# Kernel tuning notes

Measured on AMD Instinct MI355X. Metric: run time of the kernel, lower is better.

The kernel has to match this reference:

```python
import jax, jax.numpy as jnp
import numpy as np

BLOCKS = 32
BLOCK_SIZE = 8
CONV_SHAPES = [(128, 96), (128, 128), (96, 128)] * 2  # per-block conv (out,in) list


def build_conv_meta():
    meta = []
    w_total = 0
    b_total = 0
    for _ in range(BLOCKS):
        for oc, ic in CONV_SHAPES:
            meta.append((oc, ic, w_total, b_total))
            w_total += oc * ic * 9
            b_total += oc
    return meta, w_total, b_total

CONV_META, W_TOTAL, B_TOTAL = build_conv_meta()


def build_program():
    ops = [[0, 0, 0, 0], [1, 0, 0, 0], [2, 0, 0, 0]]
    for blk in range(BLOCKS):
        ops.append([3, 0, 1, 2])  # SPLIT r0 -> (r1, r2)
        for rnd in range(2):
            ci = blk * 6 + rnd * 3
            ops += [
                [4, 3, 2, ci],      # r3 = conv(r2)        128<-96
                [5, 3, 3, 0],       # r3 = relu(r3)
                [4, 3, 3, ci + 1],  # r3 = conv(r3)        128<-128
                [5, 3, 3, 0],       # r3 = relu(r3)
                [4, 3, 3, ci + 2],  # r3 = conv(r3)        96<-128
                [6, 1, 1, 3],       # r1 = r1 + r3
                [9, 1, 2, 0],       # swap(r1, r2)  (Feistel)
            ]
        ops += [[7, 0, 1, 2],       # r0 = concat(r1, r2)
                [8, 0, 0, blk]]     # r0 = mix[blk] @ r0 (1x1 conv)
    return np.array(ops, dtype=np.int64)


def space_to_depth(x, blk):
    b, c, h, w = x.shape
    x = x.reshape(b, c, h // blk, blk, w // blk, blk)
    x = jnp.transpose(x, (0, 1, 3, 5, 2, 4))
    return x.reshape(b, c * blk * blk, h // blk, w // blk)


def conv3x3(x, w, b):
    y = jax.lax.conv_general_dilated(
        x, w, window_strides=(1, 1), padding=[(1, 1), (1, 1)],
        dimension_numbers=('NCHW', 'OIHW', 'NCHW'))
    return y + b[None, :, None, None]


def run_program(x, mu, sigma, w_flat, b_flat, m, perm, ops):
    regs = [x, None, None, None, None]
    for row in np.asarray(ops):
        op, a, b, c = (int(v) for v in row)
        if op == 0:  # AFFINE
            regs[a] = (regs[a] - mu[None, :, None, None]) / sigma[None, :, None, None]
        elif op == 1:  # PERM: gather along flattened HW per channel
            bs, ch, h, w = regs[a].shape
            v = regs[a].reshape(bs, ch, h * w)
            regs[a] = jnp.take_along_axis(v, perm[None], axis=2).reshape(bs, ch, h, w)
        elif op == 2:  # S2D
            regs[a] = space_to_depth(regs[a], BLOCK_SIZE)
        elif op == 3:  # SPLIT
            regs[b], regs[c] = jnp.split(regs[a], 2, axis=1)
        elif op == 4:  # CONV (weights sliced from flat buffer, static offsets)
            oc, ic, woff, boff = CONV_META[c]
            w = w_flat[woff:woff + oc * ic * 9].reshape(oc, ic, 3, 3)
            bb = b_flat[boff:boff + oc]
            regs[a] = conv3x3(regs[b], w, bb)
        elif op == 5:  # RELU
            regs[a] = jax.nn.relu(regs[b])
        elif op == 6:  # ADD
            regs[a] = regs[b] + regs[c]
        elif op == 7:  # CONCAT
            regs[a] = jnp.concatenate([regs[b], regs[c]], axis=1)
        elif op == 8:  # MIX: 1x1 conv with 192x192 orthogonal matrix
            regs[a] = jnp.einsum('oc,bchw->bohw', m[c], regs[b])
        elif op == 9:  # SWAP
            regs[a], regs[b] = regs[b], regs[a]
        else:
            raise ValueError('bad op')
    return regs[0]


def setup_inputs() -> dict:
    key = jax.random.key(0)
    k_x, k_w, k_b = jax.random.split(key, 3)
    rng = np.random.default_rng(0)

    x = jax.random.normal(k_x, (8, 3, 256, 256), dtype=jnp.float32)
    mu = jnp.full((3,), 0.45, dtype=jnp.float32)
    sigma = jnp.full((3,), 0.2, dtype=jnp.float32)
    # conv weights ~ He-ish scale so activations stay bounded across 64 Feistel rounds
    w_flat = jax.random.normal(k_w, (W_TOTAL,), dtype=jnp.float32) * 0.04
    b_flat = jax.random.normal(k_b, (B_TOTAL,), dtype=jnp.float32) * 0.01
    # orthogonal 192x192 mix matrices per block (as in nn.init.orthogonal_)
    ms = []
    for _ in range(BLOCKS):
        q, r = np.linalg.qr(rng.standard_normal((192, 192)))
        q = q * np.sign(np.diag(r))[None, :]
        ms.append(q.astype(np.float32))
    m = jnp.asarray(np.stack(ms))  # [BLOCKS,192,192]
    # per-channel spatial permutation on the 256x256 input
    perm = jnp.asarray(np.stack([rng.permutation(256 * 256) for _ in range(3)]).astype(np.int32))
    ops = build_program()  # static numpy tape
    return {'x': x, 'mu': mu, 'sigma': sigma, 'w_flat': w_flat, 'b_flat': b_flat,
            'm': m, 'perm': perm, 'ops': ops}


def reference(x, mu, sigma, w_flat, b_flat, m, perm, ops):
    return run_program(x, mu, sigma, w_flat, b_flat, m, perm, ops)
```

## Files before the change

kernel.cpp:

```cpp
#include <hip/hip_runtime.h>

typedef _Float16 f16;
typedef _Float16 f16x8 __attribute__((ext_vector_type(8)));
typedef _Float16 f16x4 __attribute__((ext_vector_type(4)));
typedef float    f32x4 __attribute__((ext_vector_type(4)));

#define TPB 256

__global__ __launch_bounds__(TPB) void prologue_k(
    const float* __restrict__ x, const float* __restrict__ mu,
    const float* __restrict__ sigma, const int* __restrict__ perm,
    f16* __restrict__ A0)
{
    int gid = blockIdx.x * TPB + threadIdx.x;
    if (gid >= 8192 * 192) return;
    int c = gid % 192;
    int p = gid / 192;
    int b  = p >> 10;
    int h2 = (p >> 5) & 31;
    int w2 = p & 31;
    int cc = c >> 6;
    int bh = (c >> 3) & 7;
    int bw = c & 7;
    int j   = (h2 * 8 + bh) * 256 + (w2 * 8 + bw);
    int src = perm[cc * 65536 + j];
    float v = (x[(b * 3 + cc) * 65536 + src] - mu[cc]) / sigma[cc];
    A0[gid] = (f16)v;
}

__global__ __launch_bounds__(TPB) void wconv_k(const float* __restrict__ wf,
                                               f16* __restrict__ wh)
{
    int c   = blockIdx.y;
    int idx = blockIdx.x * TPB + threadIdx.x;
    int s   = c % 6;
    int s3  = s % 3;
    int oc  = (s3 == 2) ? 96 : 128;
    int ic  = (s3 == 0) ? 96 : 128;
    int wo  = (s3 == 0 ? 0 : (s3 == 1 ? 110592 : 258048)) + (s >= 3 ? 368640 : 0);
    int ocic = oc * ic;
    int n    = ocic * 9;
    if (idx >= n) return;
    size_t base = (size_t)(c / 6) * 737280 + wo;
    int tap = idx / ocic;
    int r   = idx - tap * ocic;
    int o   = r / ic;
    int i   = r - o * ic;
    wh[base + idx] = (f16)wf[base + (size_t)o * ic * 9 + (size_t)i * 9 + tap];
}

__global__ __launch_bounds__(TPB) void mconv_k(const float* __restrict__ mf,
                                               f16* __restrict__ mh, int n)
{
    int i = blockIdx.x * TPB + threadIdx.x;
    if (i < n) mh[i] = (f16)mf[i];
}

__global__ __launch_bounds__(TPB) void bconv_k(const float* __restrict__ bf,
                                               float* __restrict__ bs, int n)
{
    int i = blockIdx.x * TPB + threadIdx.x;
    if (i < n) bs[i] = ldexpf(bf[i], -(i / 704));
}

template<int IC, int OC, int TAPS, bool RELU, bool ACCUM, bool OUT32>
__global__ __launch_bounds__(TPB) void conv_k(
    const f16* __restrict__ Xin, int ICS,
    const f16* __restrict__ W,  const float* __restrict__ bias,
    f16* __restrict__ Out, int OCS, float* __restrict__ Out32, float scale)
{
    constexpr int R    = 4;
    constexpr int NC8  = IC / 8;
    constexpr int PAD  = (TAPS == 9) ? 1 : 0;
    constexpr int ROWS = R + 2 * PAD;
    constexpr int WW   = 32 + 2 * PAD;

    extern __shared__ f16 lds[];
    f16* Alds = lds + ROWS * NC8 * WW * 8;

    const int tid  = threadIdx.x;
    const int tile = blockIdx.x;
    const int img  = tile >> 3;
    const int r0   = (tile & 7) * R;
    const int oc0  = blockIdx.y * 32;

    for (int i = tid; i < ROWS * WW * NC8; i += TPB) {
        int c8  = i % NC8;
        int rem = i / NC8;
        int wv  = rem % WW;
        int ri  = rem / WW;
        int row = r0 - PAD + ri;
        int wc  = wv - PAD;
        f16x8 v = {};
        if ((unsigned)row < 32u && (unsigned)wc < 32u) {
            int p = img * 1024 + row * 32 + wc;
            v = *(const f16x8*)&Xin[(size_t)p * ICS + c8 * 8];
        }
        *(f16x8*)&lds[((ri * NC8 + c8) * WW + wv) * 8] = v;
    }

    const int lane = tid & 63;
    const int wave = tid >> 6;
    const int lq   = lane >> 4;
    const int ln   = lane & 15;

    f32x4 acc[2][2] = {};

    for (int tap = 0; tap < TAPS; ++tap) {
        __syncthreads();
        for (int i = tid; i < 32 * NC8; i += TPB) {
            int o  = i & 31;
            int c8 = i >> 5;
            *(f16x8*)&Alds[(c8 * 32 + o) * 8] =
                *(const f16x8*)&W[((size_t)tap * OC + oc0 + o) * IC + c8 * 8];
        }
        __syncthreads();

        const int dy = (TAPS == 9) ? tap / 3 - 1 : 0;
        const int dx = (TAPS == 9) ? tap % 3 - 1 : 0;
        const int bb = ((wave + PAD + dy) * NC8 * WW + (ln + dx + PAD)) * 8;

#pragma unroll
        for (int kc = 0; kc < IC / 32; ++kc) {
            f16x8 a0 = *(const f16x8*)&Alds[((kc * 4 + lq) * 32 + ln) * 8];
            f16x8 a1 = *(const f16x8*)&Alds[((kc * 4 + lq) * 32 + 16 + ln) * 8];
            f16x8 b0 = *(const f16x8*)&lds[bb + (kc * 4 + lq) * WW * 8];
            f16x8 b1 = *(const f16x8*)&lds[bb + (kc * 4 + lq) * WW * 8 + 128];
            acc[0][0] = __builtin_amdgcn_mfma_f32_16x16x32_f16(a0, b0, acc[0][0], 0, 0, 0);
            acc[1][0] = __builtin_amdgcn_mfma_f32_16x16x32_f16(a1, b0, acc[1][0], 0, 0, 0);
            acc[0][1] = __builtin_amdgcn_mfma_f32_16x16x32_f16(a0, b1, acc[0][1], 0, 0, 0);
            acc[1][1] = __builtin_amdgcn_mfma_f32_16x16x32_f16(a1, b1, acc[1][1], 0, 0, 0);
        }
    }

    const int prow = r0 + wave;
#pragma unroll
    for (int mm = 0; mm < 2; ++mm) {
#pragma unroll
        for (int nn = 0; nn < 2; ++nn) {
            int oc = oc0 + mm * 16 + lq * 4;
            int p  = img * 1024 + prow * 32 + nn * 16 + ln;
            float b0 = 0.f, b1 = 0.f, b2 = 0.f, b3 = 0.f;
            if (TAPS == 9) {
                float4 bv = *(const float4*)&bias[oc];
                b0 = bv.x; b1 = bv.y; b2 = bv.z; b3 = bv.w;
            }
            float v0 = acc[mm][nn][0] * scale + b0;
            float v1 = acc[mm][nn][1] * scale + b1;
            float v2 = acc[mm][nn][2] * scale + b2;
            float v3 = acc[mm][nn][3] * scale + b3;
            if (RELU) {
                v0 = fmaxf(v0, 0.f); v1 = fmaxf(v1, 0.f);
                v2 = fmaxf(v2, 0.f); v3 = fmaxf(v3, 0.f);
            }
            if (OUT32) {
                size_t ob = (size_t)(img * 192 + oc) * 1024 + prow * 32 + nn * 16 + ln;
                Out32[ob]          = v0;
                Out32[ob + 1024]   = v1;
                Out32[ob + 2048]   = v2;
                Out32[ob + 3072]   = v3;
            } else {
                f16* op = &Out[(size_t)p * OCS + oc];
                if (ACCUM) {
                    f16x4 old = *(const f16x4*)op;
                    v0 += (float)old[0]; v1 += (float)old[1];
                    v2 += (float)old[2]; v3 += (float)old[3];
                }
                f16x4 hv;
                hv[0] = (f16)v0; hv[1] = (f16)v1; hv[2] = (f16)v2; hv[3] = (f16)v3;
                *(f16x4*)op = hv;
            }
        }
    }
}

extern "C" void kernel_launch(void* const* d_in, const int* in_sizes, int n_in,
                              void* d_out, int out_size, void* d_ws, size_t ws_size,
                              hipStream_t stream)
{
    const float* x     = (const float*)d_in[0];
    const float* mu    = (const float*)d_in[1];
    const float* sigma = (const float*)d_in[2];
    const float* wf    = (const float*)d_in[3];
    const float* bf    = (const float*)d_in[4];
    const float* mf    = (const float*)d_in[5];
    const int*   perm  = (const int*)d_in[6];
    float*       out   = (float*)d_out;

    char* ws = (char*)d_ws;
    f16*   WH = (f16*)(ws);
    f16*   MH = (f16*)(ws + 47185920);
    float* BS = (float*)(ws + 49545216);
    f16*   XA = (f16*)(ws + 49635328);
    f16*   XB = (f16*)(ws + 52781056);
    f16*   H1 = (f16*)(ws + 55926784);
    f16*   H2 = (f16*)(ws + 58023936);

    wconv_k<<<dim3(576, 192), TPB, 0, stream>>>(wf, WH);
    mconv_k<<<dim3(4608), TPB, 0, stream>>>(mf, MH, 1179648);
    bconv_k<<<dim3(88),   TPB, 0, stream>>>(bf, BS, 22528);
    prologue_k<<<dim3(6144), TPB, 0, stream>>>(x, mu, sigma, perm, XA);

    static const int wo6[6] = {0, 110592, 258048, 368640, 479232, 626688};
    static const int bo6[6] = {0, 128, 256, 352, 480, 608};

    constexpr int LDS96  = (6 * 12 * 34 * 8 + 96 * 32) * 2;
    constexpr int LDS128 = (6 * 16 * 34 * 8 + 128 * 32) * 2;
    constexpr int LDS192 = (4 * 24 * 32 * 8 + 192 * 32) * 2;

    f16* cur = XA;
    f16* nxt = XB;
    for (int blk = 0; blk < 32; ++blk) {
        int c = blk * 6;
        size_t w0 = (size_t)blk * 737280;
        size_t b0 = (size_t)blk * 704;
        conv_k<96, 128, 9, true,  false, false><<<dim3(64, 4), TPB, LDS96, stream>>>(
            cur + 96, 192, WH + w0 + wo6[0], BS + b0 + bo6[0], H1, 128, nullptr, 1.0f);
        conv_k<128, 128, 9, true,  false, false><<<dim3(64, 4), TPB, LDS128, stream>>>(
            H1, 128, WH + w0 + wo6[1], BS + b0 + bo6[1], H2, 128, nullptr, 1.0f);
        conv_k<128, 96, 9, false, true,  false><<<dim3(64, 3), TPB, LDS128, stream>>>(
            H2, 128, WH + w0 + wo6[2], BS + b0 + bo6[2], cur, 192, nullptr, 1.0f);
        conv_k<96, 128, 9, true,  false, false><<<dim3(64, 4), TPB, LDS96, stream>>>(
            cur, 192, WH + w0 + wo6[3], BS + b0 + bo6[3], H1, 128, nullptr, 1.0f);
        conv_k<128, 128, 9, true,  false, false><<<dim3(64, 4), TPB, LDS128, stream>>>(
            H1, 128, WH + w0 + wo6[4], BS + b0 + bo6[4], H2, 128, nullptr, 1.0f);
        conv_k<128, 96, 9, false, true,  false><<<dim3(64, 3), TPB, LDS128, stream>>>(
            H2, 128, WH + w0 + wo6[5], BS + b0 + bo6[5], cur + 96, 192, nullptr, 1.0f);
        if (blk < 31) {
            conv_k<192, 192, 1, false, false, false><<<dim3(64, 6), TPB, LDS192, stream>>>(
                cur, 192, MH + (size_t)blk * 36864, nullptr, nxt, 192, nullptr, 0.5f);
        } else {
            conv_k<192, 192, 1, false, false, true><<<dim3(64, 6), TPB, LDS192, stream>>>(
                cur, 192, MH + (size_t)blk * 36864, nullptr, nullptr, 192, out,
                2147483648.0f );
        }
        f16* t = cur; cur = nxt; nxt = t;
    }
}
```

Before: 3.036 ms.

## Rewrite conv kernels with async LDS double-buffering, swizzle, and new weight layout

Restructures the convolution kernel so each block handles one output row with 128 threads. Input and weight chunks are streamed into double-buffered LDS through global_load_lds, with an XOR swizzle to avoid bank conflicts, and the next tap/chunk is prefetched while MFMAs run on the current one. Weight and mix-matrix conversion kernels now emit a channel-chunk-major layout packed as 8-wide vectors. The prologue is vectorised to write 8 halves per thread. Risks include lower per-block reuse from single-row tiles and heavier barrier traffic per tap.

```diff
diff --git a/kernel.cpp b/kernel.cpp
--- a/kernel.cpp
+++ b/kernel.cpp
@@ -5,161 +5,223 @@
 typedef _Float16 f16x4 __attribute__((ext_vector_type(4)));
 typedef float    f32x4 __attribute__((ext_vector_type(4)));
 
-#define TPB 256
-
-__global__ __launch_bounds__(TPB) void prologue_k(
+#define GLOAD16(gp, lp) __builtin_amdgcn_global_load_lds(                      \
+    (const __attribute__((address_space(1))) void*)(gp),                       \
+    (__attribute__((address_space(3))) void*)(lp), 16, 0, 0)
+
+__global__ __launch_bounds__(256) void prologue_k(
     const float* __restrict__ x, const float* __restrict__ mu,
     const float* __restrict__ sigma, const int* __restrict__ perm,
     f16* __restrict__ A0)
 {
-    int gid = blockIdx.x * TPB + threadIdx.x;
-    if (gid >= 8192 * 192) return;
-    int c = gid % 192;
-    int p = gid / 192;
+    int gid = blockIdx.x * 256 + threadIdx.x;
+    if (gid >= 8192 * 24) return;
+    int c8 = gid % 24;
+    int p  = gid / 24;
     int b  = p >> 10;
     int h2 = (p >> 5) & 31;
     int w2 = p & 31;
-    int cc = c >> 6;
-    int bh = (c >> 3) & 7;
-    int bw = c & 7;
-    int j   = (h2 * 8 + bh) * 256 + (w2 * 8 + bw);
-    int src = perm[cc * 65536 + j];
-    float v = (x[(b * 3 + cc) * 65536 + src] - mu[cc]) / sigma[cc];
-    A0[gid] = (f16)v;
-}
-
-__global__ __launch_bounds__(TPB) void wconv_k(const float* __restrict__ wf,
+    int cc = c8 >> 3;
+    int bh = c8 & 7;
+    const int* pm = &perm[cc * 65536 + (h2 * 8 + bh) * 256 + w2 * 8];
+    const float* xp = &x[(b * 3 + cc) * 65536];
+    float m = mu[cc], rs = 1.0f / sigma[cc];
+    f16 v[8];
+#pragma unroll
+    for (int k = 0; k < 8; ++k)
+        v[k] = (f16)((xp[pm[k]] - m) * rs);
+    *(f16x8*)&A0[(size_t)p * 192 + c8 * 8] = *(f16x8*)v;
+}
+
+__global__ __launch_bounds__(256) void wconv_k(const float* __restrict__ wf,
                                                f16* __restrict__ wh)
 {
     int c   = blockIdx.y;
-    int idx = blockIdx.x * TPB + threadIdx.x;
     int s   = c % 6;
     int s3  = s % 3;
-    int oc  = (s3 == 2) ? 96 : 128;
-    int ic  = (s3 == 0) ? 96 : 128;
+    int icr = (s3 == 0) ? 96 : 128;
+    int ocv = (s3 == 2) ? 96 : 128;
+    int nc8 = icr >> 3;
     int wo  = (s3 == 0 ? 0 : (s3 == 1 ? 110592 : 258048)) + (s >= 3 ? 368640 : 0);
-    int ocic = oc * ic;
-    int n    = ocic * 9;
-    if (idx >= n) return;
+    int idx = blockIdx.x * 256 + threadIdx.x;
+    if (idx >= nc8 * ocv) return;
+    int o  = idx % ocv;
+    int c8 = idx / ocv;
     size_t base = (size_t)(c / 6) * 737280 + wo;
-    int tap = idx / ocic;
-    int r   = idx - tap * ocic;
-    int o   = r / ic;
-    int i   = r - o * ic;
-    wh[base + idx] = (f16)wf[base + (size_t)o * ic * 9 + (size_t)i * 9 + tap];
-}
-
-__global__ __launch_bounds__(TPB) void mconv_k(const float* __restrict__ mf,
-                                               f16* __restrict__ mh, int n)
-{
-    int i = blockIdx.x * TPB + threadIdx.x;
-    if (i < n) mh[i] = (f16)mf[i];
-}
-
-__global__ __launch_bounds__(TPB) void bconv_k(const float* __restrict__ bf,
+    const float* src = &wf[base + ((size_t)o * icr + c8 * 8) * 9];
+    f16 vt[9][8];
+#pragma unroll
+    for (int k = 0; k < 8; ++k)
+#pragma unroll
+        for (int t = 0; t < 9; ++t)
+            vt[t][k] = (f16)src[k * 9 + t];
+#pragma unroll
+    for (int t = 0; t < 9; ++t)
+        *(f16x8*)&wh[base + ((size_t)(t * nc8 + c8) * ocv + o) * 8] = *(f16x8*)vt[t];
+}
+
+__global__ __launch_bounds__(256) void mconv_k(const float* __restrict__ mf,
+                                               f16* __restrict__ mh)
+{
+    int n = blockIdx.x * 256 + threadIdx.x;
+    if (n >= 32 * 24 * 192) return;
+    int o   = n % 192;
+    int t   = n / 192;
+    int i8  = t % 24;
+    int mat = t / 24;
+    const float* s = &mf[(size_t)mat * 36864 + o * 192 + i8 * 8];
+    f16 v[8];
+#pragma unroll
+    for (int k = 0; k < 8; ++k) v[k] = (f16)s[k];
+    *(f16x8*)&mh[(size_t)mat * 36864 + ((size_t)i8 * 192 + o) * 8] = *(f16x8*)v;
+}
+
+__global__ __launch_bounds__(256) void bconv_k(const float* __restrict__ bf,
                                                float* __restrict__ bs, int n)
 {
-    int i = blockIdx.x * TPB + threadIdx.x;
+    int i = blockIdx.x * 256 + threadIdx.x;
     if (i < n) bs[i] = ldexpf(bf[i], -(i / 704));
 }
 
-template<int IC, int OC, int TAPS, bool RELU, bool ACCUM, bool OUT32>
-__global__ __launch_bounds__(TPB) void conv_k(
+template<int OCW, int OCV, int NC8R, int TAPS, bool RELU, bool ACCUM, bool OUT32>
+__global__ __launch_bounds__(128) void conv_k(
     const f16* __restrict__ Xin, int ICS,
-    const f16* __restrict__ W,  const float* __restrict__ bias,
+    const f16* __restrict__ W, const float* __restrict__ bias,
     f16* __restrict__ Out, int OCS, float* __restrict__ Out32, float scale)
 {
-    constexpr int R    = 4;
-    constexpr int NC8  = IC / 8;
-    constexpr int PAD  = (TAPS == 9) ? 1 : 0;
-    constexpr int ROWS = R + 2 * PAD;
-    constexpr int WW   = 32 + 2 * PAD;
-
-    extern __shared__ f16 lds[];
-    f16* Alds = lds + ROWS * NC8 * WW * 8;
+    constexpr int PAD   = (TAPS == 9) ? 1 : 0;
+    constexpr int ROWS  = 1 + 2 * PAD;
+    constexpr int WW    = 32 + 2 * PAD;
+    constexpr int CHN   = (NC8R + 7) / 8;
+    constexpr int OCW2  = 2 * OCW;
+    constexpr int MM    = OCW / 16;
+    constexpr int XSLOT = ROWS * WW * 8;
+    constexpr int XB_   = XSLOT * 16;
+    constexpr int WSLOT = 8 * OCW2;
+    constexpr int WB_   = WSLOT * 16;
+
+    extern __shared__ char lds[];
 
     const int tid  = threadIdx.x;
+    const int lane = tid & 63, wave = tid >> 6;
+    const int lq   = lane >> 4, ln = lane & 15;
     const int tile = blockIdx.x;
-    const int img  = tile >> 3;
-    const int r0   = (tile & 7) * R;
-    const int oc0  = blockIdx.y * 32;
-
-    for (int i = tid; i < ROWS * WW * NC8; i += TPB) {
-        int c8  = i % NC8;
-        int rem = i / NC8;
-        int wv  = rem % WW;
-        int ri  = rem / WW;
-        int row = r0 - PAD + ri;
-        int wc  = wv - PAD;
-        f16x8 v = {};
-        if ((unsigned)row < 32u && (unsigned)wc < 32u) {
-            int p = img * 1024 + row * 32 + wc;
-            v = *(const f16x8*)&Xin[(size_t)p * ICS + c8 * 8];
-        }
-        *(f16x8*)&lds[((ri * NC8 + c8) * WW + wv) * 8] = v;
+    const int img  = tile >> 5, row = tile & 31;
+    const int ocg  = blockIdx.y * OCW2;
+
+    auto issueX = [&](int chunk, int par) {
+        char* xb = lds + par * XB_;
+        const int ch0 = chunk * 64;
+        for (int inst = wave; inst * 64 < XSLOT; inst += 2) {
+            int s   = inst * 64 + lane;
+            int c8p = s & 7;
+            int wr  = s >> 3;
+            int wv  = wr % WW;
+            int ri  = wr / WW;
+            int r   = row - PAD + ri;
+            int cl  = wv - PAD;
+            bool inb = (s < XSLOT) & ((unsigned)r < 32u) & ((unsigned)cl < 32u);
+            if (inb) {
+                int ch = ch0 + ((c8p ^ (wv & 7)) << 3);
+                const f16* g = &Xin[(size_t)(img * 1024 + r * 32 + cl) * ICS + ch];
+                GLOAD16(g, xb + inst * 1024);
+            } else if (s < XSLOT) {
+                *(f16x8*)(xb + (size_t)s * 16) = (f16x8){};
+            }
+        }
+    };
+
+    auto issueW = [&](int chunk, int tap, int par) {
+        char* wb = lds + 2 * XB_ + par * WB_;
+        for (int inst = wave; inst * 64 < WSLOT; inst += 2) {
+            int s     = inst * 64 + lane;
+            int c8l   = s / OCW2;
+            int ocL   = s - c8l * OCW2;
+            int c8abs = chunk * 8 + c8l;
+            if (c8abs < NC8R) {
+                const f16* g = &W[((size_t)(tap * NC8R + c8abs) * OCV + ocg + ocL) * 8];
+                GLOAD16(g, wb + inst * 1024);
+            } else {
+                *(f16x8*)(wb + (size_t)s * 16) = (f16x8){};
+            }
+        }
+    };
+
+    issueX(0, 0);
+    issueW(0, 0, 0);
+
+    f32x4 acc[MM][2] = {};
+    int wpar = 0;
+
+    for (int chunk = 0; chunk < CHN; ++chunk) {
+#pragma unroll
+        for (int tap = 0; tap < TAPS; ++tap) {
+            asm volatile("s_waitcnt vmcnt(0) lgkmcnt(0)" ::: "memory");
+            __builtin_amdgcn_s_barrier();
+            asm volatile("" ::: "memory");
+            {
+                int ntap = tap + 1, nch = chunk;
+                if (ntap == TAPS) { ntap = 0; nch++; }
+                if (nch < CHN) {
+                    if (ntap == 0) issueX(nch, nch & 1);
+                    issueW(nch, ntap, wpar ^ 1);
+                }
+            }
+            const int dy = (TAPS == 9) ? tap / 3 - 1 : 0;
+            const int dx = (TAPS == 9) ? tap % 3 - 1 : 0;
+            const char* xb = lds + (chunk & 1) * XB_;
+            const char* wb = lds + 2 * XB_ + wpar * WB_;
+#pragma unroll
+            for (int kc = 0; kc < 2; ++kc) {
+                const int kcg = kc * 4 + lq;
+                f16x8 a[MM], b[2];
+#pragma unroll
+                for (int m = 0; m < MM; ++m)
+                    a[m] = *(const f16x8*)(wb +
+                        (size_t)(kcg * OCW2 + wave * OCW + m * 16 + ln) * 16);
+#pragma unroll
+                for (int n = 0; n < 2; ++n) {
+                    int wv = n * 16 + ln + PAD + dx;
+                    b[n] = *(const f16x8*)(xb +
+                        (size_t)(((PAD + dy) * WW + wv) * 8 + (kcg ^ (wv & 7))) * 16);
+                }
+#pragma unroll
+                for (int m = 0; m < MM; ++m)
+#pragma unroll
+                    for (int n = 0; n < 2; ++n)
+                        acc[m][n] = __builtin_amdgcn_mfma_f32_16x16x32_f16(
+                            a[m], b[n], acc[m][n], 0, 0, 0);
+            }
+            wpar ^= 1;
+        }
     }
 
-    const int lane = tid & 63;
-    const int wave = tid >> 6;
-    const int lq   = lane >> 4;
-    const int ln   = lane & 15;
-
-    f32x4 acc[2][2] = {};
-
-    for (int tap = 0; tap < TAPS; ++tap) {
-        __syncthreads();
-        for (int i = tid; i < 32 * NC8; i += TPB) {
-            int o  = i & 31;
-            int c8 = i >> 5;
-            *(f16x8*)&Alds[(c8 * 32 + o) * 8] =
-                *(const f16x8*)&W[((size_t)tap * OC + oc0 + o) * IC + c8 * 8];
-        }
-        __syncthreads();
-
-        const int dy = (TAPS == 9) ? tap / 3 - 1 : 0;
-        const int dx = (TAPS == 9) ? tap % 3 - 1 : 0;
-        const int bb = ((wave + PAD + dy) * NC8 * WW + (ln + dx + PAD)) * 8;
-
-#pragma unroll
-        for (int kc = 0; kc < IC / 32; ++kc) {
-            f16x8 a0 = *(const f16x8*)&Alds[((kc * 4 + lq) * 32 + ln) * 8];
-            f16x8 a1 = *(const f16x8*)&Alds[((kc * 4 + lq) * 32 + 16 + ln) * 8];
-            f16x8 b0 = *(const f16x8*)&lds[bb + (kc * 4 + lq) * WW * 8];
-            f16x8 b1 = *(const f16x8*)&lds[bb + (kc * 4 + lq) * WW * 8 + 128];
-            acc[0][0] = __builtin_amdgcn_mfma_f32_16x16x32_f16(a0, b0, acc[0][0], 0, 0, 0);
-            acc[1][0] = __builtin_amdgcn_mfma_f32_16x16x32_f16(a1, b0, acc[1][0], 0, 0, 0);
-            acc[0][1] = __builtin_amdgcn_mfma_f32_16x16x32_f16(a0, b1, acc[0][1], 0, 0, 0);
-            acc[1][1] = __builtin_amdgcn_mfma_f32_16x16x32_f16(a1, b1, acc[1][1], 0, 0, 0);
-        }
-    }
-
-    const int prow = r0 + wave;
-#pragma unroll
-    for (int mm = 0; mm < 2; ++mm) {
-#pragma unroll
-        for (int nn = 0; nn < 2; ++nn) {
-            int oc = oc0 + mm * 16 + lq * 4;
-            int p  = img * 1024 + prow * 32 + nn * 16 + ln;
-            float b0 = 0.f, b1 = 0.f, b2 = 0.f, b3 = 0.f;
-            if (TAPS == 9) {
-                float4 bv = *(const float4*)&bias[oc];
-                b0 = bv.x; b1 = bv.y; b2 = bv.z; b3 = bv.w;
-            }
-            float v0 = acc[mm][nn][0] * scale + b0;
-            float v1 = acc[mm][nn][1] * scale + b1;
-            float v2 = acc[mm][nn][2] * scale + b2;
-            float v3 = acc[mm][nn][3] * scale + b3;
+#pragma unroll
+    for (int m = 0; m < MM; ++m) {
+        const int oc = ocg + wave * OCW + m * 16 + lq * 4;
+        float b0 = 0.f, b1 = 0.f, b2 = 0.f, b3 = 0.f;
+        if (TAPS == 9) {
+            float4 bv = *(const float4*)&bias[oc];
+            b0 = bv.x; b1 = bv.y; b2 = bv.z; b3 = bv.w;
+        }
+#pragma unroll
+        for (int n = 0; n < 2; ++n) {
+            float v0 = acc[m][n][0] * scale + b0;
+            float v1 = acc[m][n][1] * scale + b1;
+            float v2 = acc[m][n][2] * scale + b2;
+            float v3 = acc[m][n][3] * scale + b3;
             if (RELU) {
                 v0 = fmaxf(v0, 0.f); v1 = fmaxf(v1, 0.f);
                 v2 = fmaxf(v2, 0.f); v3 = fmaxf(v3, 0.f);
             }
             if (OUT32) {
-                size_t ob = (size_t)(img * 192 + oc) * 1024 + prow * 32 + nn * 16 + ln;
+                size_t ob = (size_t)(img * 192 + oc) * 1024 + row * 32 + n * 16 + ln;
                 Out32[ob]          = v0;
                 Out32[ob + 1024]   = v1;
                 Out32[ob + 2048]   = v2;
                 Out32[ob + 3072]   = v3;
             } else {
+                const int p = img * 1024 + row * 32 + n * 16 + ln;
                 f16* op = &Out[(size_t)p * OCS + oc];
                 if (ACCUM) {
                     f16x4 old = *(const f16x4*)op;
@@ -196,44 +258,38 @@
     f16*   H1 = (f16*)(ws + 55926784);
     f16*   H2 = (f16*)(ws + 58023936);
 
-    wconv_k<<<dim3(576, 192), TPB, 0, stream>>>(wf, WH);
-    mconv_k<<<dim3(4608), TPB, 0, stream>>>(mf, MH, 1179648);
-    bconv_k<<<dim3(88),   TPB, 0, stream>>>(bf, BS, 22528);
-    prologue_k<<<dim3(6144), TPB, 0, stream>>>(x, mu, sigma, perm, XA);
-
-    static const int wo6[6] = {0, 110592, 258048, 368640, 479232, 626688};
-    static const int bo6[6] = {0, 128, 256, 352, 480, 608};
-
-    constexpr int LDS96  = (6 * 12 * 34 * 8 + 96 * 32) * 2;
-    constexpr int LDS128 = (6 * 16 * 34 * 8 + 128 * 32) * 2;
-    constexpr int LDS192 = (4 * 24 * 32 * 8 + 192 * 32) * 2;
-
-    f16* cur = XA;
-    f16* nxt = XB;
+    wconv_k   <<<dim3(8, 192), 256, 0, stream>>>(wf, WH);
+    mconv_k   <<<dim3(576),    256, 0, stream>>>(mf, MH);
+    bconv_k   <<<dim3(88),     256, 0, stream>>>(bf, BS, 22528);
+    prologue_k<<<dim3(768),    256, 0, stream>>>(x, mu, sigma, perm, XA);
+
+    constexpr int LDS_C12 = 2 * 13056 + 2 * 8192;
+    constexpr int LDS_C3  = 2 * 13056 + 2 * 12288;
+    constexpr int LDS_MIX = 2 * 4096  + 2 * 8192;
+
     for (int blk = 0; blk < 32; ++blk) {
-        int c = blk * 6;
         size_t w0 = (size_t)blk * 737280;
         size_t b0 = (size_t)blk * 704;
-        conv_k<96, 128, 9, true,  false, false><<<dim3(64, 4), TPB, LDS96, stream>>>(
-            cur + 96, 192, WH + w0 + wo6[0], BS + b0 + bo6[0], H1, 128, nullptr, 1.0f);
-        conv_k<128, 128, 9, true,  false, false><<<dim3(64, 4), TPB, LDS128, stream>>>(
-            H1, 128, WH + w0 + wo6[1], BS + b0 + bo6[1], H2, 128, nullptr, 1.0f);
-        conv_k<128, 96, 9, false, true,  false><<<dim3(64, 3), TPB, LDS128, stream>>>(
-            H2, 128, WH + w0 + wo6[2], BS + b0 + bo6[2], cur, 192, nullptr, 1.0f);
-        conv_k<96, 128, 9, true,  false, false><<<dim3(64, 4), TPB, LDS96, stream>>>(
-            cur, 192, WH + w0 + wo6[3], BS + b0 + bo6[3], H1, 128, nullptr, 1.0f);
-        conv_k<128, 128, 9, true,  false, false><<<dim3(64, 4), TPB, LDS128, stream>>>(
-            H1, 128, WH + w0 + wo6[4], BS + b0 + bo6[4], H2, 128, nullptr, 1.0f);
-        conv_k<128, 96, 9, false, true,  false><<<dim3(64, 3), TPB, LDS128, stream>>>(
-            H2, 128, WH + w0 + wo6[5], BS + b0 + bo6[5], cur + 96, 192, nullptr, 1.0f);
-        if (blk < 31) {
-            conv_k<192, 192, 1, false, false, false><<<dim3(64, 6), TPB, LDS192, stream>>>(
+        f16* cur = (blk & 1) ? XB : XA;
+        f16* nxt = (blk & 1) ? XA : XB;
+        conv_k<32, 128, 12, 9, true,  false, false><<<dim3(256, 2), 128, LDS_C12, stream>>>(
+            cur + 96, 192, WH + w0 + 0,      BS + b0 + 0,   H1, 128, nullptr, 1.f);
+        conv_k<32, 128, 16, 9, true,  false, false><<<dim3(256, 2), 128, LDS_C12, stream>>>(
+            H1, 128,       WH + w0 + 110592, BS + b0 + 128, H2, 128, nullptr, 1.f);
+        conv_k<48,  96, 16, 9, false, true,  false><<<dim3(256, 1), 128, LDS_C3, stream>>>(
+            H2, 128,       WH + w0 + 258048, BS + b0 + 256, cur, 192, nullptr, 1.f);
+        conv_k<32, 128, 12, 9, true,  false, false><<<dim3(256, 2), 128, LDS_C12, stream>>>(
+            cur, 192,      WH + w0 + 368640, BS + b0 + 352, H1, 128, nullptr, 1.f);
+        conv_k<32, 128, 16, 9, true,  false, false><<<dim3(256, 2), 128, LDS_C12, stream>>>(
+            H1, 128,       WH + w0 + 479232, BS + b0 + 480, H2, 128, nullptr, 1.f);
+        conv_k<48,  96, 16, 9, false, true,  false><<<dim3(256, 1), 128, LDS_C3, stream>>>(
+            H2, 128,       WH + w0 + 626688, BS + b0 + 608, cur + 96, 192, nullptr, 1.f);
+        if (blk < 31)
+            conv_k<32, 192, 24, 1, false, false, false><<<dim3(256, 3), 128, LDS_MIX, stream>>>(
                 cur, 192, MH + (size_t)blk * 36864, nullptr, nxt, 192, nullptr, 0.5f);
-        } else {
-            conv_k<192, 192, 1, false, false, true><<<dim3(64, 6), TPB, LDS192, stream>>>(
+        else
+            conv_k<32, 192, 24, 1, false, false, true><<<dim3(256, 3), 128, LDS_MIX, stream>>>(
                 cur, 192, MH + (size_t)blk * 36864, nullptr, nullptr, 192, out,
-                2147483648.0f );
-        }
-        f16* t = cur; cur = nxt; nxt = t;
+                2147483648.f );
     }
 }
```

Result: slower. 3.709 ms (+22.2%).
